# Optimization experiments

Measured on AMD Instinct MI355X. Metric: run time of the kernel, lower is better.

Reference implementation:

```python
import jax, jax.numpy as jnp
import numpy as np

NUM_ROUTERS = 8
K = 2
IN_DIM = 384
HID = 64
TEMP = 1.0
AUX_COEF = 0.05
EPS = 1e-12


def _l2norm(v, axis=-1):
    n = jnp.sqrt(jnp.sum(v * v, axis=axis, keepdims=True))
    return v / jnp.maximum(n, EPS)


def setup_inputs() -> dict:
    key = jax.random.key(0)
    ks = jax.random.split(key, 10)
    B, E = 8192, 1024
    s = 1.0 / np.sqrt(IN_DIM)
    return {
        "x": jax.random.normal(ks[0], (B, IN_DIM), jnp.float32),
        "reasoning_embeddings": jax.random.normal(ks[1], (E, IN_DIM), jnp.float32),
        "random_num": jax.random.uniform(ks[2], (B, 1), jnp.float32),
        "gate_w": jax.random.normal(ks[3], (IN_DIM, NUM_ROUTERS), jnp.float32) * s,
        "gate_b": jnp.zeros((NUM_ROUTERS,), jnp.float32),
        "Uw": jax.random.normal(ks[4], (NUM_ROUTERS, IN_DIM, HID), jnp.float32) * s,
        "Ub": jnp.zeros((NUM_ROUTERS, HID), jnp.float32),
        "Vw": jax.random.normal(ks[5], (NUM_ROUTERS, IN_DIM, HID), jnp.float32) * s,
        "Vb": jnp.zeros((NUM_ROUTERS, HID), jnp.float32),
    }


def reference(x, reasoning_embeddings, random_num, gate_w, gate_b, Uw, Ub, Vw, Vb):
    B = x.shape[0]
    # gate
    logits = x @ gate_w + gate_b                              # [B, R]
    probs = jax.nn.softmax(logits, axis=-1)
    topk_vals, topk_idxs = jax.lax.top_k(logits, K)           # [B, K]
    topk_mask = jax.nn.one_hot(topk_idxs, NUM_ROUTERS).sum(axis=1)  # [B, R]
    aux_loss = NUM_ROUTERS * (probs.mean(0) * topk_mask.mean(0)).sum() * AUX_COEF

    # all routers, batched (replaces the per-(i,j) python loop)
    xu = _l2norm(jnp.einsum("bd,rdh->rbh", x, Uw) + Ub[:, None, :])          # [R, B, H]
    ev = _l2norm(jnp.einsum("ed,rdh->reh", reasoning_embeddings, Vw) + Vb[:, None, :])  # [R, E, H]
    scores = jnp.einsum("rbh,reh->rbe", xu, ev)               # [R, B, E]
    all_out = jax.nn.softmax(scores / TEMP, axis=-1)          # [R, B, E]

    # gather top-k experts per sample
    all_out_b = jnp.transpose(all_out, (1, 0, 2))             # [B, R, E]
    router_outputs = jnp.take_along_axis(all_out_b, topk_idxs[:, :, None], axis=1)  # [B, K, E]

    gate_weights = jax.nn.softmax(topk_vals, axis=-1)[:, :, None]  # [B, K, 1]
    rea_probs = jnp.sum(router_outputs * gate_weights, axis=1)     # [B, E]

    # categorical sampling via inverse-CDF
    scores_cumsum = jnp.cumsum(rea_probs, axis=1)
    selected_index = jnp.argmax((scores_cumsum > random_num).astype(jnp.float32), axis=1)  # [B]
    log_probs = jnp.log(rea_probs[jnp.arange(B), selected_index])[:, None]  # [B, 1]
    return selected_index, log_probs, aux_loss
```

## Files before the change

### kernel.cpp

```cpp
#include <hip/hip_runtime.h>
#include <math.h>

#define B 8192
#define E 1024
#define D 384
#define H 64
#define R 8
#define NCHUNK 16
#define CHUNK_E 64
#define NPOS 17408
#define NROW 25600

#define WS_COUNTS   0u
#define WS_CURSORS  32u
#define WS_PS       64u
#define WS_TOP2     256u
#define WS_GW       65792u
#define WS_POSMAP   131328u
#define WS_LIST     196864u
#define WS_EVN      266496u
#define WS_C        2363648u
#define WS_BUFA     3477760u
#define WS_BUFB     10031360u

__global__ __launch_bounds__(256) void k_gate(
    const float* __restrict__ x, const float* __restrict__ gate_w,
    const float* __restrict__ gate_b, int2* __restrict__ top2,
    float2* __restrict__ gwv, int* __restrict__ counts, float* __restrict__ ps)
{
  __shared__ __align__(16) float gwT[R * 388];
  __shared__ float psl[R];
  __shared__ int   cl[R];
  int tid = threadIdx.x;
  for (int idx = tid; idx < D * R; idx += 256) {
    int k = idx >> 3, r = idx & 7;
    gwT[r * 388 + k] = gate_w[idx];
  }
  if (tid < R) { psl[tid] = 0.f; cl[tid] = 0; }
  __syncthreads();

  int l = tid & 63;
  int r = tid & 7;
  int b = blockIdx.x * 32 + (tid >> 3);
  float acc = gate_b[r];
  const float4* x4 = (const float4*)(x + (size_t)b * D);
  const float*  gr = gwT + r * 388;
#pragma unroll 4
  for (int q = 0; q < 96; ++q) {
    float4 xv = x4[q];
    float4 gv = *(const float4*)&gr[q * 4];
    acc = fmaf(xv.x, gv.x, acc);
    acc = fmaf(xv.y, gv.y, acc);
    acc = fmaf(xv.z, gv.z, acc);
    acc = fmaf(xv.w, gv.w, acc);
  }
  float lv[R];
#pragma unroll
  for (int rr = 0; rr < R; ++rr) lv[rr] = __shfl(acc, (l & ~7) + rr);
  int i0 = 0; float v0 = lv[0];
#pragma unroll
  for (int rr = 1; rr < R; ++rr) if (lv[rr] > v0) { v0 = lv[rr]; i0 = rr; }
  int i1 = (i0 == 0) ? 1 : 0; float v1 = lv[i1];
#pragma unroll
  for (int rr = 0; rr < R; ++rr)
    if (rr != i0 && lv[rr] > v1) { v1 = lv[rr]; i1 = rr; }
  float se = 0.f;
#pragma unroll
  for (int rr = 0; rr < R; ++rr) se += expf(lv[rr] - v0);
  float p = expf(acc - v0) / se;
  if (r == 0) {
    float e10 = expf(v1 - v0);
    top2[b] = make_int2(i0, i1);
    gwv[b]  = make_float2(1.f / (1.f + e10), e10 / (1.f + e10));
  }
  float pa = p;
  int   ca = (r == i0 ? 1 : 0) + (r == i1 ? 1 : 0);
#pragma unroll
  for (int m = 8; m < 64; m <<= 1) {
    pa += __shfl_xor(pa, m);
    ca += __shfl_xor(ca, m);
  }
  if (l < 8) { atomicAdd(&psl[r], pa); atomicAdd(&cl[r], ca); }
  __syncthreads();
  if (tid < R) { atomicAdd(&ps[tid], psl[tid]); atomicAdd(&counts[tid], cl[tid]); }
}

__global__ __launch_bounds__(256) void k_scatter(
    const int2* __restrict__ top2, const int* __restrict__ counts,
    const float* __restrict__ ps, int* __restrict__ cursors,
    int* __restrict__ list, int2* __restrict__ posmap, float* __restrict__ out_aux)
{
  __shared__ int lc[R];
  __shared__ int lbase[R];
  __shared__ int offs[R];
  int tid = threadIdx.x;
  if (tid < R) lc[tid] = 0;
  __syncthreads();
  if (tid == 0) {
    int o = 0;
    for (int r2 = 0; r2 < R; ++r2) { offs[r2] = o; o += (min(counts[r2], B) + 127) & ~127; }
  }
  __syncthreads();
  int b = min(blockIdx.x * 256 + tid, B - 1);
  int2 t = top2[b];
  t.x &= 7; t.y &= 7;
  int p0 = atomicAdd(&lc[t.x], 1);
  int p1 = atomicAdd(&lc[t.y], 1);
  __syncthreads();
  if (tid < R) lbase[tid] = atomicAdd(&cursors[tid], lc[tid]);
  __syncthreads();
  int i0 = min(offs[t.x] + lbase[t.x] + p0, NPOS - 1);
  int i1 = min(offs[t.y] + lbase[t.y] + p1, NPOS - 1);
  list[i0] = b * 2 + 0;
  list[i1] = b * 2 + 1;
  posmap[b] = make_int2(i0, i1);
  if (blockIdx.x == 0 && tid == 0) {
    float s = 0.f;
    for (int r2 = 0; r2 < R; ++r2)
      s += (ps[r2] / (float)B) * ((float)min(counts[r2], B) / (float)B);
    out_aux[0] = (float)R * s * 0.05f;
  }
}

__global__ __launch_bounds__(128) void k_projgemm(
    const float* __restrict__ re, const float* __restrict__ x,
    const float* __restrict__ Vw, const float* __restrict__ Uw,
    const int* __restrict__ list, const int* __restrict__ counts,
    float* __restrict__ bufA, float* __restrict__ bufB)
{
  __shared__ __align__(16) float At[64 * 128];
  __shared__ __align__(16) float Wt[64 * 64];
  int tid = threadIdx.x;
  int bid = blockIdx.x;
  int tile = bid >> 1, ks = bid & 1;

  int srow = tid;
  const float* Wsrc;
  const float* arow;
  int rowg0;
  if (tile < 64) {
    int r = tile >> 3;
    rowg0 = tile * 128;
    Wsrc = Vw + (size_t)r * (D * H);
    arow = re + (size_t)((tile * 128 & 1023) + srow) * D;
  } else {
    int pos0 = (tile - 64) * 128;
    int tot = 0, r = 0;
    for (int rr = 0; rr < R; ++rr) {
      int seg = (min(counts[rr], B) + 127) & ~127;
      if (pos0 >= tot) r = rr;
      tot += seg;
    }
    if (pos0 >= tot) return;
    rowg0 = 8192 + pos0;
    Wsrc = Uw + (size_t)r * (D * H);
    int gl = list[min(pos0 + srow, NPOS - 1)];
    gl = min(max(gl, 0), 2 * B - 1);
    arow = x + (size_t)(gl >> 1) * D;
  }

  int sg = tid >> 3, hg = tid & 7;
  float acc[8][8];
#pragma unroll
  for (int i = 0; i < 8; ++i)
#pragma unroll
    for (int j = 0; j < 8; ++j) acc[i][j] = 0.f;

  for (int kt = 0; kt < 3; ++kt) {
    int kb = ks * 192 + kt * 64;
    __syncthreads();
#pragma unroll
    for (int q = 0; q < 16; ++q) {
      float4 v = *(const float4*)&arow[kb + q * 4];
      At[(q * 4 + 0) * 128 + srow] = v.x;
      At[(q * 4 + 1) * 128 + srow] = v.y;
      At[(q * 4 + 2) * 128 + srow] = v.z;
      At[(q * 4 + 3) * 128 + srow] = v.w;
    }
#pragma unroll
    for (int q = 0; q < 8; ++q) {
      int idx = tid + 128 * q;
      int k = idx >> 4, h4 = idx & 15;
      *(float4*)&Wt[k * 64 + h4 * 4] = *(const float4*)&Wsrc[(size_t)(kb + k) * H + h4 * 4];
    }
    __syncthreads();
#pragma unroll 8
    for (int k = 0; k < 64; ++k) {
      float4 xa = *(const float4*)&At[k * 128 + sg * 4];
      float4 xb = *(const float4*)&At[k * 128 + 64 + sg * 4];
      float4 wa = *(const float4*)&Wt[k * 64 + hg * 4];
      float4 wb = *(const float4*)&Wt[k * 64 + 32 + hg * 4];
      const float* pa = (const float*)&xa;
      const float* pb = (const float*)&xb;
      const float* qa = (const float*)&wa;
      const float* qb = (const float*)&wb;
#pragma unroll
      for (int i = 0; i < 4; ++i)
#pragma unroll
        for (int j = 0; j < 4; ++j) {
          acc[i][j]         = fmaf(pa[i], qa[j], acc[i][j]);
          acc[i][j + 4]     = fmaf(pa[i], qb[j], acc[i][j + 4]);
          acc[i + 4][j]     = fmaf(pb[i], qa[j], acc[i + 4][j]);
          acc[i + 4][j + 4] = fmaf(pb[i], qb[j], acc[i + 4][j + 4]);
        }
    }
  }
  float* dst = (ks ? bufB : bufA) + (size_t)rowg0 * H;
#pragma unroll
  for (int i = 0; i < 8; ++i) {
    int rl = (i < 4) ? (sg * 4 + i) : (64 + sg * 4 + i - 4);
    float4 o0, o1;
    o0.x = acc[i][0]; o0.y = acc[i][1]; o0.z = acc[i][2]; o0.w = acc[i][3];
    o1.x = acc[i][4]; o1.y = acc[i][5]; o1.z = acc[i][6]; o1.w = acc[i][7];
    *(float4*)&dst[rl * H + hg * 4]      = o0;
    *(float4*)&dst[rl * H + 32 + hg * 4] = o1;
  }
}

__global__ __launch_bounds__(256) void k_evnfin(
    const float* __restrict__ bufA, const float* __restrict__ bufB,
    const float* __restrict__ Vb, float* __restrict__ evnT)
{
  int tid = threadIdx.x;
  int lane = tid & 63;
  int row0 = blockIdx.x * 32 + (tid >> 6) * 8;
  int r = row0 >> 10;
  float bias = Vb[r * H + lane];
#pragma unroll
  for (int i = 0; i < 8; ++i) {
    int row = row0 + i;
    float s = bufA[(size_t)row * H + lane] + bufB[(size_t)row * H + lane] + bias;
    float ss = s * s;
#pragma unroll
    for (int m = 1; m < 64; m <<= 1) ss += __shfl_xor(ss, m);
    float v = s / fmaxf(sqrtf(ss), 1e-12f);
    evnT[(size_t)(r * 64 + lane) * 1024 + (row & 1023)] = v;
  }
}

__global__ __launch_bounds__(256) void k_pass1(
    const float* __restrict__ evnT, const float* __restrict__ bufA,
    const float* __restrict__ bufB, const float* __restrict__ Ub,
    const int* __restrict__ counts, float* __restrict__ C)
{
  __shared__ __align__(16) float Xt[64 * 128];
  __shared__ __align__(16) float Et[64 * 128];
  __shared__ int cntL[R];
  int tid = threadIdx.x;
  if (tid < R) cntL[tid] = min(counts[tid], B);
  __syncthreads();

  int bid = blockIdx.x;
  int et    = bid & 7;
  int stile = (bid >> 3) & 63;
  int r     = bid >> 9;
  int cnt = cntL[r];
  if (cnt <= 0 || stile * 128 >= cnt) return;
  int off = 0;
  for (int rr = 0; rr < r; ++rr) off += (cntL[rr] + 127) & ~127;
  off += stile * 128;
  int n = min(128, cnt - stile * 128);
  int ebase = et * 128;

  {
    int row = tid >> 1, half = tid & 1;
    int rc  = min(row, n - 1);
    const float4* pA = (const float4*)(bufA + (size_t)(8192 + off + rc) * H) + half * 8;
    const float4* pB = (const float4*)(bufB + (size_t)(8192 + off + rc) * H) + half * 8;
    const float4* pU = (const float4*)(Ub + r * H) + half * 8;
    float v[32]; float ss = 0.f;
#pragma unroll
    for (int q = 0; q < 8; ++q) {
      float4 a = pA[q], bq = pB[q], u = pU[q];
      float4 w;
      w.x = a.x + bq.x + u.x; w.y = a.y + bq.y + u.y;
      w.z = a.z + bq.z + u.z; w.w = a.w + bq.w + u.w;
      v[q*4+0] = w.x; v[q*4+1] = w.y; v[q*4+2] = w.z; v[q*4+3] = w.w;
      ss = fmaf(w.x, w.x, ss); ss = fmaf(w.y, w.y, ss);
      ss = fmaf(w.z, w.z, ss); ss = fmaf(w.w, w.w, ss);
    }
    ss += __shfl_xor(ss, 1);
    float rn = 1.f / fmaxf(sqrtf(ss), 1e-12f);
#pragma unroll
    for (int q = 0; q < 32; ++q)
      Xt[(half * 32 + q) * 128 + row] = v[q] * rn;
  }
  {
#pragma unroll
    for (int q = 0; q < 8; ++q) {
      int idx = tid + 256 * q;
      int h = idx >> 5, e4 = idx & 31;
      *(float4*)&Et[h * 128 + e4 * 4] =
          *(const float4*)(evnT + (size_t)(r * 64 + h) * 1024 + ebase + e4 * 4);
    }
  }
  __syncthreads();

  int sg = tid >> 4, egr = tid & 15;
  float acc[8][8];
#pragma unroll
  for (int i = 0; i < 8; ++i)
#pragma unroll
    for (int j = 0; j < 8; ++j) acc[i][j] = 0.f;

#pragma unroll 4
  for (int k = 0; k < 64; ++k) {
    float4 xa = *(const float4*)&Xt[k * 128 + sg * 4];
    float4 xb = *(const float4*)&Xt[k * 128 + 64 + sg * 4];
    float4 ea = *(const float4*)&Et[k * 128 + egr * 4];
    float4 eb = *(const float4*)&Et[k * 128 + 64 + egr * 4];
    const float* pa = (const float*)&xa;
    const float* pb = (const float*)&xb;
    const float* qa = (const float*)&ea;
    const float* qb = (const float*)&eb;
#pragma unroll
    for (int i = 0; i < 4; ++i)
#pragma unroll
      for (int j = 0; j < 4; ++j) {
        acc[i][j]         = fmaf(pa[i], qa[j], acc[i][j]);
        acc[i][j + 4]     = fmaf(pa[i], qb[j], acc[i][j + 4]);
        acc[i + 4][j]     = fmaf(pb[i], qa[j], acc[i + 4][j]);
        acc[i + 4][j + 4] = fmaf(pb[i], qb[j], acc[i + 4][j + 4]);
      }
  }

#pragma unroll
  for (int i = 0; i < 8; ++i) {
    float cA = expf(acc[i][0]) + expf(acc[i][1]) + expf(acc[i][2]) + expf(acc[i][3]);
    float cB = expf(acc[i][4]) + expf(acc[i][5]) + expf(acc[i][6]) + expf(acc[i][7]);
#pragma unroll
    for (int m = 1; m < 16; m <<= 1) {
      cA += __shfl_xor(cA, m);
      cB += __shfl_xor(cB, m);
    }
    int s = (i < 4) ? (sg * 4 + i) : (64 + sg * 4 + i - 4);
    if (egr == 0 && s < n) {
      C[(size_t)(off + s) * NCHUNK + et * 2]     = cA;
      C[(size_t)(off + s) * NCHUNK + et * 2 + 1] = cB;
    }
  }
}

__global__ __launch_bounds__(256) void k_pass2(
    const float* __restrict__ evnT, const float* __restrict__ bufA,
    const float* __restrict__ bufB, const float* __restrict__ Ub,
    const float* __restrict__ C, const int2* __restrict__ top2,
    const int2* __restrict__ posmap, const float2* __restrict__ gwv,
    const float* __restrict__ rnd, float* __restrict__ out)
{
  int tid = threadIdx.x;
  int lane = tid & 63;
  int b = blockIdx.x * 4 + (tid >> 6);
  if (b >= B) return;
  int2 t2 = top2[b];
  t2.x &= 7; t2.y &= 7;
  int2 pm = posmap[b];
  pm.x = min(max(pm.x, 0), NPOS - 1);
  pm.y = min(max(pm.y, 0), NPOS - 1);
  float2 gw = gwv[b];
  float rv = rnd[b];

  const float4* C04 = (const float4*)(C + (size_t)pm.x * NCHUNK);
  const float4* C14 = (const float4*)(C + (size_t)pm.y * NCHUNK);
  float c0[NCHUNK], c1[NCHUNK];
#pragma unroll
  for (int q = 0; q < 4; ++q) {
    float4 v0 = C04[q], v1 = C14[q];
    c0[q*4+0]=v0.x; c0[q*4+1]=v0.y; c0[q*4+2]=v0.z; c0[q*4+3]=v0.w;
    c1[q*4+0]=v1.x; c1[q*4+1]=v1.y; c1[q*4+2]=v1.z; c1[q*4+3]=v1.w;
  }
  float S0 = 0.f, S1 = 0.f;
#pragma unroll
  for (int j = 0; j < NCHUNK; ++j) { S0 += c0[j]; S1 += c1[j]; }
  float a0 = gw.x / S0, a1 = gw.y / S1;
  int cstar = -1; float prefix = 0.f; float run = 0.f;
#pragma unroll
  for (int j = 0; j < NCHUNK; ++j) {
    float nrun = run + (c0[j] * a0 + c1[j] * a1);
    if (cstar < 0 && nrun > rv) { cstar = j; prefix = run; }
    run = nrun;
  }
  float rtgt = rv;
  if (cstar < 0) { cstar = 0; prefix = 0.f; rtgt = -1.0f; }

  float v0x = bufA[(size_t)(8192 + pm.x) * H + lane] +
              bufB[(size_t)(8192 + pm.x) * H + lane] + Ub[t2.x * H + lane];
  float v1x = bufA[(size_t)(8192 + pm.y) * H + lane] +
              bufB[(size_t)(8192 + pm.y) * H + lane] + Ub[t2.y * H + lane];
  float s0 = v0x * v0x, s1 = v1x * v1x;
#pragma unroll
  for (int m = 1; m < 64; m <<= 1) { s0 += __shfl_xor(s0, m); s1 += __shfl_xor(s1, m); }
  float xu0 = v0x / fmaxf(sqrtf(s0), 1e-12f);
  float xu1 = v1x / fmaxf(sqrtf(s1), 1e-12f);

  const float* E0 = evnT + (size_t)t2.x * 64 * 1024 + cstar * CHUNK_E + lane;
  const float* E1 = evnT + (size_t)t2.y * 64 * 1024 + cstar * CHUNK_E + lane;
  float d0 = 0.f, d1 = 0.f;
#pragma unroll 16
  for (int h = 0; h < 64; ++h) {
    float w0 = __shfl(xu0, h);
    float w1 = __shfl(xu1, h);
    d0 = fmaf(E0[(size_t)h * 1024], w0, d0);
    d1 = fmaf(E1[(size_t)h * 1024], w1, d1);
  }
  float rea = expf(d0) * a0 + expf(d1) * a1;
  float sc = rea;
#pragma unroll
  for (int d = 1; d < 64; d <<= 1) {
    float o = __shfl_up(sc, d);
    if (lane >= d) sc += o;
  }
  float cum = prefix + sc;
  unsigned long long m2 = __ballot(cum > rtgt);
  int estar = (m2 == 0ull) ? 63 : (int)__builtin_ctzll(m2);
  float p = __shfl(rea, estar);
  if (lane == 0) {
    int sel = cstar * CHUNK_E + estar;
    out[b]     = (float)sel;
    out[B + b] = logf(p);
  }
}

extern "C" void kernel_launch(void* const* d_in, const int* in_sizes, int n_in,
                              void* d_out, int out_size, void* d_ws, size_t ws_size,
                              hipStream_t stream)
{
  (void)in_sizes; (void)n_in; (void)out_size; (void)ws_size;
  const float* x      = (const float*)d_in[0];
  const float* re     = (const float*)d_in[1];
  const float* rnd    = (const float*)d_in[2];
  const float* gate_w = (const float*)d_in[3];
  const float* gate_b = (const float*)d_in[4];
  const float* Uw     = (const float*)d_in[5];
  const float* Ub     = (const float*)d_in[6];
  const float* Vw     = (const float*)d_in[7];
  const float* Vb     = (const float*)d_in[8];
  char* ws = (char*)d_ws;
  int*    counts  = (int*)(ws + WS_COUNTS);
  int*    cursors = (int*)(ws + WS_CURSORS);
  float*  ps      = (float*)(ws + WS_PS);
  int2*   top2    = (int2*)(ws + WS_TOP2);
  float2* gwv     = (float2*)(ws + WS_GW);
  int2*   posmap  = (int2*)(ws + WS_POSMAP);
  int*    list    = (int*)(ws + WS_LIST);
  float*  evnT    = (float*)(ws + WS_EVN);
  float*  Cc      = (float*)(ws + WS_C);
  float*  bufA    = (float*)(ws + WS_BUFA);
  float*  bufB    = (float*)(ws + WS_BUFB);
  float* out = (float*)d_out;

  hipMemsetAsync(ws, 0, 256, stream);
  k_gate    <<<256,  256, 0, stream>>>(x, gate_w, gate_b, top2, gwv, counts, ps);
  k_scatter <<<32,   256, 0, stream>>>(top2, counts, ps, cursors, list, posmap, out + 2 * B);
  k_projgemm<<<400,  128, 0, stream>>>(re, x, Vw, Uw, list, counts, bufA, bufB);
  k_evnfin  <<<256,  256, 0, stream>>>(bufA, bufB, Vb, evnT);
  k_pass1   <<<4096, 256, 0, stream>>>(evnT, bufA, bufB, Ub, counts, Cc);
  k_pass2   <<<2048, 256, 0, stream>>>(evnT, bufA, bufB, Ub, Cc, top2, posmap, gwv, rnd, out);
}
```

Baseline: 194.4 us.

## Precompute normalized xu once, replace global atomics with per-block counts, shrink smem tiles

The gate kernel now writes per-block counts and probability sums instead of doing global atomics. The scatter kernel derives deterministic prefix offsets from those, which also removes the memset. The x-side projection finalization (bias add and L2 normalize) moves into a combined projfin kernel that writes a normalized xun buffer, so pass1 and pass2 no longer recompute normalization from bufA and bufB. The projgemm and pass1 shared-memory tiles are halved with more k-steps to raise occupancy, at the cost of extra syncs and an extra intermediate buffer.

Result: slower. 223.7 us (+15.1%).

```diff
diff --git a/kernel.cpp b/kernel.cpp
--- a/kernel.cpp
+++ b/kernel.cpp
@@ -11,22 +11,24 @@
 #define NPOS 17408
 #define NROW 25600
 
-#define WS_COUNTS   0u
-#define WS_CURSORS  32u
-#define WS_PS       64u
-#define WS_TOP2     256u
-#define WS_GW       65792u
-#define WS_POSMAP   131328u
-#define WS_LIST     196864u
-#define WS_EVN      266496u
-#define WS_C        2363648u
-#define WS_BUFA     3477760u
-#define WS_BUFB     10031360u
+#define WS_GCNT   0u
+#define WS_GPS    8192u
+#define WS_CNT    16384u
+#define WS_OFFS   16416u
+#define WS_TOP2   16448u
+#define WS_GW     81984u
+#define WS_POSM   147520u
+#define WS_LIST   213056u
+#define WS_EVN    282688u
+#define WS_XUN    2379840u
+#define WS_C      6836288u
+#define WS_BUFA   7950400u
+#define WS_BUFB   14504000u
 
 __global__ __launch_bounds__(256) void k_gate(
     const float* __restrict__ x, const float* __restrict__ gate_w,
     const float* __restrict__ gate_b, int2* __restrict__ top2,
-    float2* __restrict__ gwv, int* __restrict__ counts, float* __restrict__ ps)
+    float2* __restrict__ gwv, int* __restrict__ gcnt, float* __restrict__ gps)
 {
   __shared__ __align__(16) float gwT[R * 388];
   __shared__ float psl[R];
@@ -82,42 +84,58 @@
   }
   if (l < 8) { atomicAdd(&psl[r], pa); atomicAdd(&cl[r], ca); }
   __syncthreads();
-  if (tid < R) { atomicAdd(&ps[tid], psl[tid]); atomicAdd(&counts[tid], cl[tid]); }
-}
-
-__global__ __launch_bounds__(256) void k_scatter(
-    const int2* __restrict__ top2, const int* __restrict__ counts,
-    const float* __restrict__ ps, int* __restrict__ cursors,
+  if (tid < R) {
+    gcnt[blockIdx.x * R + tid] = cl[tid];
+    gps [blockIdx.x * R + tid] = psl[tid];
+  }
+}
+
+__global__ __launch_bounds__(64) void k_scatter(
+    const int2* __restrict__ top2, const int* __restrict__ gcnt,
+    const float* __restrict__ gps, int* __restrict__ counts, int* __restrict__ offs_g,
     int* __restrict__ list, int2* __restrict__ posmap, float* __restrict__ out_aux)
 {
-  __shared__ int lc[R];
-  __shared__ int lbase[R];
-  __shared__ int offs[R];
-  int tid = threadIdx.x;
-  if (tid < R) lc[tid] = 0;
+  __shared__ int cnt[R], pre[R], offs[R], lc[R];
+  int tid = threadIdx.x;
+  int g = blockIdx.x;
+  if (tid < R) {
+    int c = 0, pr = 0;
+    for (int gg = 0; gg < 256; ++gg) {
+      int v = gcnt[gg * R + tid];
+      c += v;
+      if (gg < g) pr += v;
+    }
+    cnt[tid] = min(c, B);
+    pre[tid] = pr;
+    lc[tid] = 0;
+  }
   __syncthreads();
   if (tid == 0) {
     int o = 0;
-    for (int r2 = 0; r2 < R; ++r2) { offs[r2] = o; o += (min(counts[r2], B) + 127) & ~127; }
+    for (int r2 = 0; r2 < R; ++r2) { offs[r2] = o; o += (cnt[r2] + 127) & ~127; }
   }
   __syncthreads();
-  int b = min(blockIdx.x * 256 + tid, B - 1);
-  int2 t = top2[b];
-  t.x &= 7; t.y &= 7;
-  int p0 = atomicAdd(&lc[t.x], 1);
-  int p1 = atomicAdd(&lc[t.y], 1);
-  __syncthreads();
-  if (tid < R) lbase[tid] = atomicAdd(&cursors[tid], lc[tid]);
-  __syncthreads();
-  int i0 = min(offs[t.x] + lbase[t.x] + p0, NPOS - 1);
-  int i1 = min(offs[t.y] + lbase[t.y] + p1, NPOS - 1);
-  list[i0] = b * 2 + 0;
-  list[i1] = b * 2 + 1;
-  posmap[b] = make_int2(i0, i1);
-  if (blockIdx.x == 0 && tid == 0) {
+  if (tid < 32) {
+    int b = g * 32 + tid;
+    int2 t = top2[b];
+    t.x &= 7; t.y &= 7;
+    int p0 = atomicAdd(&lc[t.x], 1);
+    int p1 = atomicAdd(&lc[t.y], 1);
+    int i0 = min(offs[t.x] + pre[t.x] + p0, NPOS - 1);
+    int i1 = min(offs[t.y] + pre[t.y] + p1, NPOS - 1);
+    list[i0] = b * 2 + 0;
+    list[i1] = b * 2 + 1;
+    posmap[b] = make_int2(i0, i1);
+  }
+  if (g == 0 && tid == 0) {
     float s = 0.f;
-    for (int r2 = 0; r2 < R; ++r2)
-      s += (ps[r2] / (float)B) * ((float)min(counts[r2], B) / (float)B);
+    for (int r2 = 0; r2 < R; ++r2) {
+      float pssum = 0.f;
+      for (int gg = 0; gg < 256; ++gg) pssum += gps[gg * R + r2];
+      s += (pssum / (float)B) * ((float)cnt[r2] / (float)B);
+      counts[r2] = cnt[r2];
+      offs_g[r2] = offs[r2];
+    }
     out_aux[0] = (float)R * s * 0.05f;
   }
 }
@@ -128,21 +146,19 @@
     const int* __restrict__ list, const int* __restrict__ counts,
     float* __restrict__ bufA, float* __restrict__ bufB)
 {
-  __shared__ __align__(16) float At[64 * 128];
-  __shared__ __align__(16) float Wt[64 * 64];
+  __shared__ __align__(16) float At[32 * 128];
+  __shared__ __align__(16) float Wt[32 * 64];
   int tid = threadIdx.x;
   int bid = blockIdx.x;
   int tile = bid >> 1, ks = bid & 1;
 
-  int srow = tid;
   const float* Wsrc;
   const float* arow;
   int rowg0;
   if (tile < 64) {
-    int r = tile >> 3;
     rowg0 = tile * 128;
-    Wsrc = Vw + (size_t)r * (D * H);
-    arow = re + (size_t)((tile * 128 & 1023) + srow) * D;
+    Wsrc = Vw + (size_t)(rowg0 >> 10) * (D * H);
+    arow = re + (size_t)((rowg0 & 1023) + tid) * D;
   } else {
     int pos0 = (tile - 64) * 128;
     int tot = 0, r = 0;
@@ -154,40 +170,40 @@
     if (pos0 >= tot) return;
     rowg0 = 8192 + pos0;
     Wsrc = Uw + (size_t)r * (D * H);
-    int gl = list[min(pos0 + srow, NPOS - 1)];
+    int gl = list[min(pos0 + tid, NPOS - 1)];
     gl = min(max(gl, 0), 2 * B - 1);
     arow = x + (size_t)(gl >> 1) * D;
   }
 
-  int sg = tid >> 3, hg = tid & 7;
+  int rg = tid >> 3, hg = tid & 7;
   float acc[8][8];
 #pragma unroll
   for (int i = 0; i < 8; ++i)
 #pragma unroll
     for (int j = 0; j < 8; ++j) acc[i][j] = 0.f;
 
-  for (int kt = 0; kt < 3; ++kt) {
-    int kb = ks * 192 + kt * 64;
+  for (int kt = 0; kt < 6; ++kt) {
+    int kb = ks * 192 + kt * 32;
     __syncthreads();
 #pragma unroll
-    for (int q = 0; q < 16; ++q) {
+    for (int q = 0; q < 8; ++q) {
       float4 v = *(const float4*)&arow[kb + q * 4];
-      At[(q * 4 + 0) * 128 + srow] = v.x;
-      At[(q * 4 + 1) * 128 + srow] = v.y;
-      At[(q * 4 + 2) * 128 + srow] = v.z;
-      At[(q * 4 + 3) * 128 + srow] = v.w;
-    }
-#pragma unroll
-    for (int q = 0; q < 8; ++q) {
+      At[(q * 4 + 0) * 128 + tid] = v.x;
+      At[(q * 4 + 1) * 128 + tid] = v.y;
+      At[(q * 4 + 2) * 128 + tid] = v.z;
+      At[(q * 4 + 3) * 128 + tid] = v.w;
+    }
+#pragma unroll
+    for (int q = 0; q < 4; ++q) {
       int idx = tid + 128 * q;
       int k = idx >> 4, h4 = idx & 15;
       *(float4*)&Wt[k * 64 + h4 * 4] = *(const float4*)&Wsrc[(size_t)(kb + k) * H + h4 * 4];
     }
     __syncthreads();
 #pragma unroll 8
-    for (int k = 0; k < 64; ++k) {
-      float4 xa = *(const float4*)&At[k * 128 + sg * 4];
-      float4 xb = *(const float4*)&At[k * 128 + 64 + sg * 4];
+    for (int k = 0; k < 32; ++k) {
+      float4 xa = *(const float4*)&At[k * 128 + rg * 4];
+      float4 xb = *(const float4*)&At[k * 128 + 64 + rg * 4];
       float4 wa = *(const float4*)&Wt[k * 64 + hg * 4];
       float4 wb = *(const float4*)&Wt[k * 64 + 32 + hg * 4];
       const float* pa = (const float*)&xa;
@@ -208,7 +224,7 @@
   float* dst = (ks ? bufB : bufA) + (size_t)rowg0 * H;
 #pragma unroll
   for (int i = 0; i < 8; ++i) {
-    int rl = (i < 4) ? (sg * 4 + i) : (64 + sg * 4 + i - 4);
+    int rl = (i < 4) ? (rg * 4 + i) : (64 + rg * 4 + i - 4);
     float4 o0, o1;
     o0.x = acc[i][0]; o0.y = acc[i][1]; o0.z = acc[i][2]; o0.w = acc[i][3];
     o1.x = acc[i][4]; o1.y = acc[i][5]; o1.z = acc[i][6]; o1.w = acc[i][7];
@@ -217,15 +233,24 @@
   }
 }
 
-__global__ __launch_bounds__(256) void k_evnfin(
+__global__ __launch_bounds__(256) void k_projfin(
     const float* __restrict__ bufA, const float* __restrict__ bufB,
-    const float* __restrict__ Vb, float* __restrict__ evnT)
+    const float* __restrict__ Vb, const float* __restrict__ Ub,
+    const int* __restrict__ offs, float* __restrict__ evnT,
+    float* __restrict__ xunP)
 {
   int tid = threadIdx.x;
   int lane = tid & 63;
   int row0 = blockIdx.x * 32 + (tid >> 6) * 8;
-  int r = row0 >> 10;
-  float bias = Vb[r * H + lane];
+  bool isE = row0 < 8192;
+  int r = 0;
+  if (isE) {
+    r = row0 >> 10;
+  } else {
+    int pos = row0 - 8192;
+    for (int rr = 0; rr < R; ++rr) if (pos >= offs[rr]) r = rr;
+  }
+  float bias = isE ? Vb[r * H + lane] : Ub[r * H + lane];
 #pragma unroll
   for (int i = 0; i < 8; ++i) {
     int row = row0 + i;
@@ -234,68 +259,29 @@
 #pragma unroll
     for (int m = 1; m < 64; m <<= 1) ss += __shfl_xor(ss, m);
     float v = s / fmaxf(sqrtf(ss), 1e-12f);
-    evnT[(size_t)(r * 64 + lane) * 1024 + (row & 1023)] = v;
+    if (isE) evnT[(size_t)(r * 64 + lane) * 1024 + (row & 1023)] = v;
+    else     xunP[(size_t)(row - 8192) * H + lane] = v;
   }
 }
 
 __global__ __launch_bounds__(256) void k_pass1(
-    const float* __restrict__ evnT, const float* __restrict__ bufA,
-    const float* __restrict__ bufB, const float* __restrict__ Ub,
-    const int* __restrict__ counts, float* __restrict__ C)
-{
-  __shared__ __align__(16) float Xt[64 * 128];
-  __shared__ __align__(16) float Et[64 * 128];
-  __shared__ int cntL[R];
-  int tid = threadIdx.x;
-  if (tid < R) cntL[tid] = min(counts[tid], B);
-  __syncthreads();
-
+    const float* __restrict__ evnT, const float* __restrict__ xunP,
+    const int* __restrict__ counts, const int* __restrict__ offs,
+    float* __restrict__ C)
+{
+  __shared__ __align__(16) float Xt[32 * 128];
+  __shared__ __align__(16) float Et[32 * 128];
+  int tid = threadIdx.x;
   int bid = blockIdx.x;
   int et    = bid & 7;
   int stile = (bid >> 3) & 63;
   int r     = bid >> 9;
-  int cnt = cntL[r];
+  int cnt = min(counts[r], B);
   if (cnt <= 0 || stile * 128 >= cnt) return;
-  int off = 0;
-  for (int rr = 0; rr < r; ++rr) off += (cntL[rr] + 127) & ~127;
-  off += stile * 128;
+  int off = offs[r] + stile * 128;
   int n = min(128, cnt - stile * 128);
   int ebase = et * 128;
 
-  {
-    int row = tid >> 1, half = tid & 1;
-    int rc  = min(row, n - 1);
-    const float4* pA = (const float4*)(bufA + (size_t)(8192 + off + rc) * H) + half * 8;
-    const float4* pB = (const float4*)(bufB + (size_t)(8192 + off + rc) * H) + half * 8;
-    const float4* pU = (const float4*)(Ub + r * H) + half * 8;
-    float v[32]; float ss = 0.f;
-#pragma unroll
-    for (int q = 0; q < 8; ++q) {
-      float4 a = pA[q], bq = pB[q], u = pU[q];
-      float4 w;
-      w.x = a.x + bq.x + u.x; w.y = a.y + bq.y + u.y;
-      w.z = a.z + bq.z + u.z; w.w = a.w + bq.w + u.w;
-      v[q*4+0] = w.x; v[q*4+1] = w.y; v[q*4+2] = w.z; v[q*4+3] = w.w;
-      ss = fmaf(w.x, w.x, ss); ss = fmaf(w.y, w.y, ss);
-      ss = fmaf(w.z, w.z, ss); ss = fmaf(w.w, w.w, ss);
-    }
-    ss += __shfl_xor(ss, 1);
-    float rn = 1.f / fmaxf(sqrtf(ss), 1e-12f);
-#pragma unroll
-    for (int q = 0; q < 32; ++q)
-      Xt[(half * 32 + q) * 128 + row] = v[q] * rn;
-  }
-  {
-#pragma unroll
-    for (int q = 0; q < 8; ++q) {
-      int idx = tid + 256 * q;
-      int h = idx >> 5, e4 = idx & 31;
-      *(float4*)&Et[h * 128 + e4 * 4] =
-          *(const float4*)(evnT + (size_t)(r * 64 + h) * 1024 + ebase + e4 * 4);
-    }
-  }
-  __syncthreads();
-
   int sg = tid >> 4, egr = tid & 15;
   float acc[8][8];
 #pragma unroll
@@ -303,25 +289,53 @@
 #pragma unroll
     for (int j = 0; j < 8; ++j) acc[i][j] = 0.f;
 
+  int srow = tid >> 1, shalf = tid & 1;
+  int src = min(srow, n - 1);
+  const float4* xsrc = (const float4*)(xunP + (size_t)(off + src) * H);
+
+  for (int kst = 0; kst < 2; ++kst) {
+    __syncthreads();
+    {
+#pragma unroll
+      for (int q = 0; q < 4; ++q) {
+        float4 v = xsrc[kst * 8 + shalf * 4 + q];
+        int hb = shalf * 16 + q * 4;
+        Xt[(hb + 0) * 128 + srow] = v.x;
+        Xt[(hb + 1) * 128 + srow] = v.y;
+        Xt[(hb + 2) * 128 + srow] = v.z;
+        Xt[(hb + 3) * 128 + srow] = v.w;
+      }
+    }
+    {
+#pragma unroll
+      for (int q = 0; q < 4; ++q) {
+        int idx = tid + 256 * q;
+        int h = idx >> 5, e4 = idx & 31;
+        *(float4*)&Et[h * 128 + e4 * 4] =
+            *(const float4*)(evnT + (size_t)(r * 64 + kst * 32 + h) * 1024 + ebase + e4 * 4);
+      }
+    }
+    __syncthreads();
 #pragma unroll 4
-  for (int k = 0; k < 64; ++k) {
-    float4 xa = *(const float4*)&Xt[k * 128 + sg * 4];
-    float4 xb = *(const float4*)&Xt[k * 128 + 64 + sg * 4];
-    float4 ea = *(const float4*)&Et[k * 128 + egr * 4];
-    float4 eb = *(const float4*)&Et[k * 128 + 64 + egr * 4];
-    const float* pa = (const float*)&xa;
-    const float* pb = (const float*)&xb;
-    const float* qa = (const float*)&ea;
-    const float* qb = (const float*)&eb;
-#pragma unroll
-    for (int i = 0; i < 4; ++i)
-#pragma unroll
-      for (int j = 0; j < 4; ++j) {
-        acc[i][j]         = fmaf(pa[i], qa[j], acc[i][j]);
-        acc[i][j + 4]     = fmaf(pa[i], qb[j], acc[i][j + 4]);
-        acc[i + 4][j]     = fmaf(pb[i], qa[j], acc[i + 4][j]);
-        acc[i + 4][j + 4] = fmaf(pb[i], qb[j], acc[i + 4][j + 4]);
-      }
+    for (int k = 0; k < 32; ++k) {
+      float4 xa = *(const float4*)&Xt[k * 128 + sg * 4];
+      float4 xb = *(const float4*)&Xt[k * 128 + 64 + sg * 4];
+      float4 ea = *(const float4*)&Et[k * 128 + egr * 4];
+      float4 eb = *(const float4*)&Et[k * 128 + 64 + egr * 4];
+      const float* pa = (const float*)&xa;
+      const float* pb = (const float*)&xb;
+      const float* qa = (const float*)&ea;
+      const float* qb = (const float*)&eb;
+#pragma unroll
+      for (int i = 0; i < 4; ++i)
+#pragma unroll
+        for (int j = 0; j < 4; ++j) {
+          acc[i][j]         = fmaf(pa[i], qa[j], acc[i][j]);
+          acc[i][j + 4]     = fmaf(pa[i], qb[j], acc[i][j + 4]);
+          acc[i + 4][j]     = fmaf(pb[i], qa[j], acc[i + 4][j]);
+          acc[i + 4][j + 4] = fmaf(pb[i], qb[j], acc[i + 4][j + 4]);
+        }
+    }
   }
 
 #pragma unroll
@@ -342,8 +356,7 @@
 }
 
 __global__ __launch_bounds__(256) void k_pass2(
-    const float* __restrict__ evnT, const float* __restrict__ bufA,
-    const float* __restrict__ bufB, const float* __restrict__ Ub,
+    const float* __restrict__ evnT, const float* __restrict__ xunP,
     const float* __restrict__ C, const int2* __restrict__ top2,
     const int2* __restrict__ posmap, const float2* __restrict__ gwv,
     const float* __restrict__ rnd, float* __restrict__ out)
@@ -383,16 +396,8 @@
   float rtgt = rv;
   if (cstar < 0) { cstar = 0; prefix = 0.f; rtgt = -1.0f; }
 
-  float v0x = bufA[(size_t)(8192 + pm.x) * H + lane] +
-              bufB[(size_t)(8192 + pm.x) * H + lane] + Ub[t2.x * H + lane];
-  float v1x = bufA[(size_t)(8192 + pm.y) * H + lane] +
-              bufB[(size_t)(8192 + pm.y) * H + lane] + Ub[t2.y * H + lane];
-  float s0 = v0x * v0x, s1 = v1x * v1x;
-#pragma unroll
-  for (int m = 1; m < 64; m <<= 1) { s0 += __shfl_xor(s0, m); s1 += __shfl_xor(s1, m); }
-  float xu0 = v0x / fmaxf(sqrtf(s0), 1e-12f);
-  float xu1 = v1x / fmaxf(sqrtf(s1), 1e-12f);
-
+  float xu0 = xunP[(size_t)pm.x * H + lane];
+  float xu1 = xunP[(size_t)pm.y * H + lane];
   const float* E0 = evnT + (size_t)t2.x * 64 * 1024 + cstar * CHUNK_E + lane;
   const float* E1 = evnT + (size_t)t2.y * 64 * 1024 + cstar * CHUNK_E + lane;
   float d0 = 0.f, d1 = 0.f;
@@ -436,24 +441,25 @@
   const float* Vw     = (const float*)d_in[7];
   const float* Vb     = (const float*)d_in[8];
   char* ws = (char*)d_ws;
-  int*    counts  = (int*)(ws + WS_COUNTS);
-  int*    cursors = (int*)(ws + WS_CURSORS);
-  float*  ps      = (float*)(ws + WS_PS);
+  int*    gcnt    = (int*)(ws + WS_GCNT);
+  float*  gps     = (float*)(ws + WS_GPS);
+  int*    counts  = (int*)(ws + WS_CNT);
+  int*    offs    = (int*)(ws + WS_OFFS);
   int2*   top2    = (int2*)(ws + WS_TOP2);
   float2* gwv     = (float2*)(ws + WS_GW);
-  int2*   posmap  = (int2*)(ws + WS_POSMAP);
+  int2*   posmap  = (int2*)(ws + WS_POSM);
   int*    list    = (int*)(ws + WS_LIST);
   float*  evnT    = (float*)(ws + WS_EVN);
+  float*  xunP    = (float*)(ws + WS_XUN);
   float*  Cc      = (float*)(ws + WS_C);
   float*  bufA    = (float*)(ws + WS_BUFA);
   float*  bufB    = (float*)(ws + WS_BUFB);
   float* out = (float*)d_out;
 
-  hipMemsetAsync(ws, 0, 256, stream);
-  k_gate    <<<256,  256, 0, stream>>>(x, gate_w, gate_b, top2, gwv, counts, ps);
-  k_scatter <<<32,   256, 0, stream>>>(top2, counts, ps, cursors, list, posmap, out + 2 * B);
+  k_gate    <<<256,  256, 0, stream>>>(x, gate_w, gate_b, top2, gwv, gcnt, gps);
+  k_scatter <<<256,  64,  0, stream>>>(top2, gcnt, gps, counts, offs, list, posmap, out + 2 * B);
   k_projgemm<<<400,  128, 0, stream>>>(re, x, Vw, Uw, list, counts, bufA, bufB);
-  k_evnfin  <<<256,  256, 0, stream>>>(bufA, bufB, Vb, evnT);
-  k_pass1   <<<4096, 256, 0, stream>>>(evnT, bufA, bufB, Ub, counts, Cc);
-  k_pass2   <<<2048, 256, 0, stream>>>(evnT, bufA, bufB, Ub, Cc, top2, posmap, gwv, rnd, out);
-}
+  k_projfin <<<800,  256, 0, stream>>>(bufA, bufB, Vb, Ub, offs, evnT, xunP);
+  k_pass1   <<<4096, 256, 0, stream>>>(evnT, xunP, counts, offs, Cc);
+  k_pass2   <<<2048, 256, 0, stream>>>(evnT, xunP, Cc, top2, posmap, gwv, rnd, out);
+}
```
